# Kernel tuning notes

Measured on AMD Instinct MI355X. Metric: run time of the kernel, lower is better.

The kernel has to match this reference:

```python
import jax, jax.numpy as jnp
import numpy as np

EMBED_DIM = 1024
NUM_HEADS = 16
HEAD_DIM = EMBED_DIM // NUM_HEADS
SCALE = HEAD_DIM ** -0.5


def setup_inputs() -> dict:
    key = jax.random.key(0)
    k_x, k_qkv, k_w, k_b = jax.random.split(key, 4)
    B, N = 2, 2048
    x = jax.random.normal(k_x, (B, N, EMBED_DIM), dtype=jnp.float32)
    # nn.Linear weights stored as (out, in); init with small normal
    w_qkv = jax.random.normal(k_qkv, (3 * EMBED_DIM, EMBED_DIM), dtype=jnp.float32) * (EMBED_DIM ** -0.5)
    w_out = jax.random.normal(k_w, (EMBED_DIM, EMBED_DIM), dtype=jnp.float32) * (EMBED_DIM ** -0.5)
    b_out = jax.random.normal(k_b, (EMBED_DIM,), dtype=jnp.float32) * 0.02
    return {"x": x, "w_qkv": w_qkv, "w_out": w_out, "b_out": b_out}


def reference(x, w_qkv, w_out, b_out):
    B, N, _ = x.shape
    # qkv: (B, N, 3*E) -> (B, N, 3, H, Dh)
    qkv = jnp.einsum('bne,fe->bnf', x, w_qkv).reshape(B, N, 3, NUM_HEADS, HEAD_DIM)
    q, k, v = qkv[:, :, 0], qkv[:, :, 1], qkv[:, :, 2]
    scores = jnp.einsum('bnhd,bmhd->bhnm', q, k) * SCALE
    attn = jax.nn.softmax(scores, axis=-1)  # dropout is identity in eval mode
    out = jnp.einsum('bhnm,bmhd->bnhd', attn, v).reshape(B, N, EMBED_DIM)
    return jnp.einsum('bne,fe->bnf', out, w_out) + b_out
```

## Files before the change

kernel.cpp:

```cpp
#include <hip/hip_runtime.h>
#include <stdint.h>
#include <stddef.h>

#define SEQ   2048
#define BATCH 2
#define NTOK  (SEQ*BATCH)
#define EMB   1024
#define QKVN  3072
#define NH    16
#define HD    64

typedef __bf16 bf16x8 __attribute__((ext_vector_type(8)));
typedef float  f32x4  __attribute__((ext_vector_type(4)));

__device__ __forceinline__ unsigned short f2b(float f) {
  union { float f; uint32_t u; } v; v.f = f;
  uint32_t r = v.u + 0x7fffu + ((v.u >> 16) & 1u);
  return (unsigned short)(r >> 16);
}

#define GLOAD_LDS16(gp, lp)                                                    \
  __builtin_amdgcn_global_load_lds(                                            \
      (__attribute__((address_space(1))) void*)(gp),                           \
      (__attribute__((address_space(3))) void*)(lp), 16, 0, 0)

__global__ void cvt3_kernel(const float* __restrict__ x,
                            const float* __restrict__ wq,
                            const float* __restrict__ wo,
                            unsigned short* __restrict__ xb,
                            unsigned short* __restrict__ wqb,
                            unsigned short* __restrict__ wob) {
  int i = blockIdx.x * blockDim.x + threadIdx.x;
  const float* in; unsigned short* out; int k;
  if (i < 1048576)              { in = x;  out = xb;  k = i; }
  else if (i < 1048576+786432)  { in = wq; out = wqb; k = i - 1048576; }
  else                          { in = wo; out = wob; k = i - (1048576+786432); }
  float4 v = ((const float4*)in)[k];
  ushort4 o;
  o.x = f2b(v.x); o.y = f2b(v.y); o.z = f2b(v.z); o.w = f2b(v.w);
  ((ushort4*)out)[k] = o;
}

__global__ __launch_bounds__(256) void gemm_bt(
    const unsigned short* __restrict__ A,
    const unsigned short* __restrict__ B,
    unsigned short* __restrict__ Cb,
    float* __restrict__ Cf,
    const float* __restrict__ bias,
    unsigned short* __restrict__ vt,
    int M, int N, int K, int mode)
{
  __shared__ unsigned short As[3][128*32];
  __shared__ unsigned short Bs[3][128*32];

  const int tid  = threadIdx.x;
  const int wave = tid >> 6, lane = tid & 63;
  const int l16  = lane & 15, quad = lane >> 4;
  const int tm = blockIdx.x * 128, tn = blockIdx.y * 128;
  const int wm = (wave & 1) * 64,  wn = (wave >> 1) * 64;

  const int e0   = (wave*2 + 0)*512 + lane*8;
  const int e1   = (wave*2 + 1)*512 + lane*8;
  const int row0 = e0 >> 5, kk0a = e0 & 31;
  const int row1 = e1 >> 5, kk1a = e1 & 31;
  const int ld0  = (wave*2 + 0)*512;
  const int ld1  = (wave*2 + 1)*512;

#define GSTAGE(bf, k0s)                                                        \
  do {                                                                         \
    GLOAD_LDS16(A + (size_t)(tm + row0)*K + ((k0s) + kk0a), As[bf] + ld0);     \
    GLOAD_LDS16(B + (size_t)(tn + row0)*K + ((k0s) + kk0a), Bs[bf] + ld0);     \
    GLOAD_LDS16(A + (size_t)(tm + row1)*K + ((k0s) + kk1a), As[bf] + ld1);     \
    GLOAD_LDS16(B + (size_t)(tn + row1)*K + ((k0s) + kk1a), Bs[bf] + ld1);     \
  } while (0)

  f32x4 acc[4][4] = {};
  const int nst = K >> 5;

  GSTAGE(0, 0);
  GSTAGE(1, 32);

  int b0i = 0, b1i = 1, b2i = 2;
  for (int t = 0; t < nst; ++t) {
    if (t + 2 < nst) GSTAGE(b2i, (t + 2)*32);

    if (t + 2 < nst)      asm volatile("s_waitcnt vmcnt(8)" ::: "memory");
    else if (t + 1 < nst) asm volatile("s_waitcnt vmcnt(4)" ::: "memory");
    else                  asm volatile("s_waitcnt vmcnt(0)" ::: "memory");
    __builtin_amdgcn_s_barrier();
    __builtin_amdgcn_sched_barrier(0);

    const unsigned short* Ac = As[b0i];
    const unsigned short* Bc = Bs[b0i];
    bf16x8 af[4], bf[4];
#pragma unroll
    for (int i = 0; i < 4; ++i) {
      af[i] = *(const bf16x8*)(Ac + (wm + i*16 + l16)*32 + quad*8);
      bf[i] = *(const bf16x8*)(Bc + (wn + i*16 + l16)*32 + quad*8);
    }
#pragma unroll
    for (int mi = 0; mi < 4; ++mi)
#pragma unroll
      for (int ni = 0; ni < 4; ++ni)
        acc[mi][ni] = __builtin_amdgcn_mfma_f32_16x16x32_bf16(af[mi], bf[ni], acc[mi][ni], 0, 0, 0);

    __builtin_amdgcn_s_barrier();
    __builtin_amdgcn_sched_barrier(0);
    const int tmp = b0i; b0i = b1i; b1i = b2i; b2i = tmp;
  }
#undef GSTAGE

  if (mode == 1) {
#pragma unroll
    for (int mi = 0; mi < 4; ++mi)
#pragma unroll
      for (int ni = 0; ni < 4; ++ni)
#pragma unroll
        for (int r = 0; r < 4; ++r) {
          const int row = tm + wm + mi*16 + quad*4 + r;
          const int col = tn + wn + ni*16 + l16;
          Cf[(size_t)row*N + col] = acc[mi][ni][r] + bias[col];
        }
  } else {
    if (tn < 2048) {
#pragma unroll
      for (int mi = 0; mi < 4; ++mi)
#pragma unroll
        for (int ni = 0; ni < 4; ++ni)
#pragma unroll
          for (int r = 0; r < 4; ++r) {
            const int row = tm + wm + mi*16 + quad*4 + r;
            const int col = tn + wn + ni*16 + l16;
            Cb[(size_t)row*2048 + col] = f2b(acc[mi][ni][r]);
          }
    } else {
#pragma unroll
      for (int mi = 0; mi < 4; ++mi)
#pragma unroll
        for (int ni = 0; ni < 4; ++ni) {
          const int f     = tn + wn + ni*16 + l16 - 2048;
          const int row0_ = tm + wm + mi*16 + quad*4;
          const int bb    = row0_ >> 11;
          const int n0    = row0_ & 2047;
          ushort4 pv;
          pv.x = f2b(acc[mi][ni][0]); pv.y = f2b(acc[mi][ni][1]);
          pv.z = f2b(acc[mi][ni][2]); pv.w = f2b(acc[mi][ni][3]);
          *(ushort4*)(vt + ((size_t)(bb*1024 + f))*2048 + n0) = pv;
        }
    }
  }
}

__global__ __launch_bounds__(256) void attn_kernel(
    const unsigned short* __restrict__ qk,
    const unsigned short* __restrict__ vT,
    unsigned short* __restrict__ aout)
{
  __shared__ unsigned short Ks[4][32*64];
  __shared__ unsigned short Vt[4][64*32];

  const int tid  = threadIdx.x;
  const int wave = tid >> 6, lane = tid & 63;
  const int l16  = lane & 15, quad = lane >> 4;

  const int flat = blockIdx.x;
  const int xcd  = flat & 7;
  const int idx  = flat >> 3;
  const int bh   = xcd*4 + (idx >> 5);
  const int qt   = idx & 31;
  const int b  = bh >> 4, h = bh & 15;
  const size_t tok0 = (size_t)b * SEQ;
  const int qrow0 = qt*64 + wave*16;
  const int ksw = l16 & 7;
  const int xsw = (l16 >> 1) & 3;

  const int p     = wave*64 + lane;
  const int krow  = p >> 3;
  const int kc    = ((p & 7) ^ (krow & 7)) << 3;
  const int vd    = p >> 2;
  const int vc    = ((p & 3) ^ ((vd >> 1) & 3)) << 3;
  const unsigned short* kbase = qk + tok0*2048 + 1024 + h*64;
  const unsigned short* vbase = vT + ((size_t)(b*1024 + h*64))*2048;
  const int ldstw = wave*512;

#define STAGE(bf, t)                                                          \
  do {                                                                        \
    const int _kk = (t)*32;                                                   \
    GLOAD_LDS16(kbase + (size_t)(_kk + krow)*2048 + kc, &Ks[bf][ldstw]);      \
    GLOAD_LDS16(vbase + (size_t)vd*2048 + _kk + vc,     &Vt[bf][ldstw]);      \
  } while (0)

  const float LOG2E = 1.44269504f;
  const float OFF2  = 17.3123405f;
#define SM_TO_PF(sReg, pfOut, lAcc)                                            \
  do {                                                                         \
    uint32_t A0_, A1_, B0_, B1_;                                               \
    float rs_ = (lAcc);                                                        \
    _Pragma("unroll")                                                          \
    for (int mf_ = 0; mf_ < 2; ++mf_) {                                        \
      union { float f; uint32_t u; } a0, a1, a2, a3;                           \
      a0.f = __builtin_amdgcn_exp2f(fmaf((sReg)[mf_][0], LOG2E, -OFF2));       \
      a1.f = __builtin_amdgcn_exp2f(fmaf((sReg)[mf_][1], LOG2E, -OFF2));       \
      a2.f = __builtin_amdgcn_exp2f(fmaf((sReg)[mf_][2], LOG2E, -OFF2));       \
      a3.f = __builtin_amdgcn_exp2f(fmaf((sReg)[mf_][3], LOG2E, -OFF2));       \
      rs_ += (a0.f + a1.f) + (a2.f + a3.f);                                    \
      uint32_t w0 = __builtin_amdgcn_perm(a1.u, a0.u, 0x07060302u);            \
      uint32_t w1 = __builtin_amdgcn_perm(a3.u, a2.u, 0x07060302u);            \
      if (mf_ == 0) { A0_ = w0; A1_ = w1; } else { B0_ = w0; B1_ = w1; }       \
    }                                                                          \
    (lAcc) = rs_;                                                              \
    asm("v_permlane32_swap_b32 %0, %1" : "+v"(A0_), "+v"(B0_));                \
    asm("v_permlane32_swap_b32 %0, %1" : "+v"(A1_), "+v"(B1_));                \
    asm("v_permlane16_swap_b32 %0, %1" : "+v"(A0_), "+v"(B0_));                \
    asm("v_permlane16_swap_b32 %0, %1" : "+v"(A1_), "+v"(B1_));                \
    union { uint32_t u[4]; bf16x8 v; } pu_;                                    \
    pu_.u[0] = A0_; pu_.u[1] = A1_; pu_.u[2] = B0_; pu_.u[3] = B1_;            \
    (pfOut) = pu_.v;                                                           \
  } while (0)

  bf16x8 qf[2];
  {
    const unsigned short* qp = qk + (tok0 + qrow0 + l16)*2048 + h*64;
#pragma unroll
    for (int ks = 0; ks < 2; ++ks) {
      bf16x8 t = *(const bf16x8*)(qp + ks*32 + quad*8);
#pragma unroll
      for (int j = 0; j < 8; ++j) t[j] = (__bf16)((float)t[j] * 0.125f);
      qf[ks] = t;
    }
  }

  f32x4 oacc[4] = {};
  float l_run = 0.f;

  STAGE(0, 0);
  STAGE(1, 1);
  __syncthreads();

#pragma unroll 2
  for (int kbb = 0; kbb < SEQ/64; ++kbb) {
    const int t0 = kbb*2;
    const int b0 = t0 & 3, b1 = (t0 + 1) & 3;
    if (t0 + 2 < SEQ/32) { STAGE((t0+2)&3, t0+2); STAGE((t0+3)&3, t0+3); }

    f32x4 sA[2] = {}, sB[2] = {};
    __builtin_amdgcn_s_setprio(1);
#pragma unroll
    for (int ks = 0; ks < 2; ++ks)
#pragma unroll
      for (int mf = 0; mf < 2; ++mf) {
        bf16x8 kf = *(const bf16x8*)(&Ks[b0][(mf*16 + l16)*64 + (((ks*4 + quad) ^ ksw) << 3)]);
        sA[mf] = __builtin_amdgcn_mfma_f32_16x16x32_bf16(kf, qf[ks], sA[mf], 0, 0, 0);
      }
#pragma unroll
    for (int ks = 0; ks < 2; ++ks)
#pragma unroll
      for (int mf = 0; mf < 2; ++mf) {
        bf16x8 kf = *(const bf16x8*)(&Ks[b1][(mf*16 + l16)*64 + (((ks*4 + quad) ^ ksw) << 3)]);
        sB[mf] = __builtin_amdgcn_mfma_f32_16x16x32_bf16(kf, qf[ks], sB[mf], 0, 0, 0);
      }
    __builtin_amdgcn_s_setprio(0);

    bf16x8 pfA;
    SM_TO_PF(sA, pfA, l_run);
    __builtin_amdgcn_s_setprio(1);
#pragma unroll
    for (int mf = 0; mf < 4; ++mf) {
      bf16x8 vf = *(const bf16x8*)(&Vt[b0][(mf*16 + l16)*32 + ((quad ^ xsw) << 3)]);
      oacc[mf] = __builtin_amdgcn_mfma_f32_16x16x32_bf16(vf, pfA, oacc[mf], 0, 0, 0);
    }
    __builtin_amdgcn_s_setprio(0);

    bf16x8 pfB;
    SM_TO_PF(sB, pfB, l_run);
    __builtin_amdgcn_s_setprio(1);
#pragma unroll
    for (int mf = 0; mf < 4; ++mf) {
      bf16x8 vf = *(const bf16x8*)(&Vt[b1][(mf*16 + l16)*32 + ((quad ^ xsw) << 3)]);
      oacc[mf] = __builtin_amdgcn_mfma_f32_16x16x32_bf16(vf, pfB, oacc[mf], 0, 0, 0);
    }
    __builtin_amdgcn_s_setprio(0);

    __syncthreads();
  }
#undef STAGE
#undef SM_TO_PF

  {
    float l = l_run;
    l += __shfl_xor(l, 16);
    l += __shfl_xor(l, 32);
    const float inv = 1.0f / l;
    const size_t trow = tok0 + qrow0 + l16;
#pragma unroll
    for (int mf = 0; mf < 4; ++mf) {
      ushort4 ov;
      ov.x = f2b(oacc[mf][0] * inv);
      ov.y = f2b(oacc[mf][1] * inv);
      ov.z = f2b(oacc[mf][2] * inv);
      ov.w = f2b(oacc[mf][3] * inv);
      *(ushort4*)(aout + trow*EMB + h*64 + mf*16 + quad*4) = ov;
    }
  }
}

extern "C" void kernel_launch(void* const* d_in, const int* in_sizes, int n_in,
                              void* d_out, int out_size, void* d_ws, size_t ws_size,
                              hipStream_t stream) {
  const float* x     = (const float*)d_in[0];
  const float* w_qkv = (const float*)d_in[1];
  const float* w_out = (const float*)d_in[2];
  const float* b_out = (const float*)d_in[3];

  char* ws = (char*)d_ws;
  unsigned short* xb    = (unsigned short*)(ws);
  unsigned short* wqkvb = (unsigned short*)(ws + 8388608);
  unsigned short* woutb = (unsigned short*)(ws + 14680064);
  unsigned short* qkb   = (unsigned short*)(ws + 16777216);
  unsigned short* vTb   = (unsigned short*)(ws + 33554432);
  unsigned short* aob   = (unsigned short*)(ws + 41943040);

  cvt3_kernel<<<8192, 256, 0, stream>>>(x, w_qkv, w_out, xb, wqkvb, woutb);

  gemm_bt<<<dim3(NTOK/128, QKVN/128), 256, 0, stream>>>(
      xb, wqkvb, qkb, nullptr, nullptr, vTb, NTOK, QKVN, EMB, 2);

  attn_kernel<<<dim3(1024), 256, 0, stream>>>(qkb, vTb, aob);

  gemm_bt<<<dim3(NTOK/128, EMB/128), 256, 0, stream>>>(
      aob, woutb, nullptr, (float*)d_out, b_out, nullptr, NTOK, EMB, EMB, 1);
}
```

Measured before the change: 188.4 us.

## Use 256x256 tiles with 512 threads and XCD-aware mapping for QKV GEMM

Adds a dedicated QKV projection GEMM kernel with 256x256 output tiles, 8 waves of 128x64 each, and a block-index remap that groups work per XCD. The larger tile roughly halves global/LDS traffic per FLOP relative to 128x128 tiles and launches 192 workgroups, fewer than the 256 CUs on the device. The out-projection GEMM is simplified to a single fp32+bias epilogue. Risks include higher register pressure (128 accumulator floats per lane), 96KB of LDS per block limiting occupancy, and some CUs left idle.

```diff
diff --git a/kernel.cpp b/kernel.cpp
--- a/kernel.cpp
+++ b/kernel.cpp
@@ -41,14 +41,108 @@
   ((ushort4*)out)[k] = o;
 }
 
+__global__ __launch_bounds__(512) void gemm256_qkv(
+    const unsigned short* __restrict__ A,
+    const unsigned short* __restrict__ B,
+    unsigned short* __restrict__ Cb,
+    unsigned short* __restrict__ vt)
+{
+  __shared__ unsigned short As[3][256*32];
+  __shared__ unsigned short Bs[3][256*32];
+
+  const int tid  = threadIdx.x;
+  const int wave = tid >> 6, lane = tid & 63;
+  const int l16  = lane & 15, quad = lane >> 4;
+  const int K = 1024;
+
+  const int flat = blockIdx.x;
+  const int wg   = (flat & 7) * 24 + (flat >> 3);
+  const int mt   = wg & 15, nt = wg >> 4;
+  const int tm   = mt * 256, tn = nt * 256;
+  const int wm   = (wave >> 2) * 128;
+  const int wn   = (wave & 3) * 64;
+
+  const int p0 = tid,        r0 = p0 >> 2, c0 = (p0 & 3) << 3;
+  const int p1 = 512 + tid,  r1 = p1 >> 2, c1 = (p1 & 3) << 3;
+
+#define GSTAGE(bf, k0s)                                                        \
+  do {                                                                         \
+    GLOAD_LDS16(A + (size_t)(tm + r0)*K + ((k0s) + c0), As[bf] + wave*512);    \
+    GLOAD_LDS16(B + (size_t)(tn + r0)*K + ((k0s) + c0), Bs[bf] + wave*512);    \
+    GLOAD_LDS16(A + (size_t)(tm + r1)*K + ((k0s) + c1), As[bf] + 4096 + wave*512); \
+    GLOAD_LDS16(B + (size_t)(tn + r1)*K + ((k0s) + c1), Bs[bf] + 4096 + wave*512); \
+  } while (0)
+
+  f32x4 acc[8][4] = {};
+
+  GSTAGE(0, 0);
+  GSTAGE(1, 32);
+
+  int b0i = 0, b1i = 1, b2i = 2;
+  for (int t = 0; t < 32; ++t) {
+    if (t + 2 < 32) GSTAGE(b2i, (t + 2)*32);
+
+    if (t + 2 < 32)      asm volatile("s_waitcnt vmcnt(8)" ::: "memory");
+    else if (t + 1 < 32) asm volatile("s_waitcnt vmcnt(4)" ::: "memory");
+    else                 asm volatile("s_waitcnt vmcnt(0)" ::: "memory");
+    __builtin_amdgcn_s_barrier();
+    __builtin_amdgcn_sched_barrier(0);
+
+    const unsigned short* Ac = As[b0i];
+    const unsigned short* Bc = Bs[b0i];
+    bf16x8 af[8], bg[4];
+#pragma unroll
+    for (int i = 0; i < 8; ++i)
+      af[i] = *(const bf16x8*)(Ac + (wm + i*16 + l16)*32 + quad*8);
+#pragma unroll
+    for (int i = 0; i < 4; ++i)
+      bg[i] = *(const bf16x8*)(Bc + (wn + i*16 + l16)*32 + quad*8);
+#pragma unroll
+    for (int mi = 0; mi < 8; ++mi)
+#pragma unroll
+      for (int ni = 0; ni < 4; ++ni)
+        acc[mi][ni] = __builtin_amdgcn_mfma_f32_16x16x32_bf16(af[mi], bg[ni], acc[mi][ni], 0, 0, 0);
+
+    __builtin_amdgcn_s_barrier();
+    __builtin_amdgcn_sched_barrier(0);
+    const int tmp = b0i; b0i = b1i; b1i = b2i; b2i = tmp;
+  }
+#undef GSTAGE
+
+  if (tn < 2048) {
+#pragma unroll
+    for (int mi = 0; mi < 8; ++mi)
+#pragma unroll
+      for (int ni = 0; ni < 4; ++ni)
+#pragma unroll
+        for (int r = 0; r < 4; ++r) {
+          const int row = tm + wm + mi*16 + quad*4 + r;
+          const int col = tn + wn + ni*16 + l16;
+          Cb[(size_t)row*2048 + col] = f2b(acc[mi][ni][r]);
+        }
+  } else {
+#pragma unroll
+    for (int mi = 0; mi < 8; ++mi)
+#pragma unroll
+      for (int ni = 0; ni < 4; ++ni) {
+        const int f     = tn + wn + ni*16 + l16 - 2048;
+        const int row0_ = tm + wm + mi*16 + quad*4;
+        const int bb    = row0_ >> 11;
+        const int n0    = row0_ & 2047;
+        ushort4 pv;
+        pv.x = f2b(acc[mi][ni][0]); pv.y = f2b(acc[mi][ni][1]);
+        pv.z = f2b(acc[mi][ni][2]); pv.w = f2b(acc[mi][ni][3]);
+        *(ushort4*)(vt + ((size_t)(bb*1024 + f))*2048 + n0) = pv;
+      }
+  }
+}
+
 __global__ __launch_bounds__(256) void gemm_bt(
     const unsigned short* __restrict__ A,
     const unsigned short* __restrict__ B,
-    unsigned short* __restrict__ Cb,
     float* __restrict__ Cf,
     const float* __restrict__ bias,
-    unsigned short* __restrict__ vt,
-    int M, int N, int K, int mode)
+    int M, int N, int K)
 {
   __shared__ unsigned short As[3][128*32];
   __shared__ unsigned short Bs[3][128*32];
@@ -110,45 +204,16 @@
   }
 #undef GSTAGE
 
-  if (mode == 1) {
-#pragma unroll
-    for (int mi = 0; mi < 4; ++mi)
-#pragma unroll
-      for (int ni = 0; ni < 4; ++ni)
-#pragma unroll
-        for (int r = 0; r < 4; ++r) {
-          const int row = tm + wm + mi*16 + quad*4 + r;
-          const int col = tn + wn + ni*16 + l16;
-          Cf[(size_t)row*N + col] = acc[mi][ni][r] + bias[col];
-        }
-  } else {
-    if (tn < 2048) {
-#pragma unroll
-      for (int mi = 0; mi < 4; ++mi)
-#pragma unroll
-        for (int ni = 0; ni < 4; ++ni)
-#pragma unroll
-          for (int r = 0; r < 4; ++r) {
-            const int row = tm + wm + mi*16 + quad*4 + r;
-            const int col = tn + wn + ni*16 + l16;
-            Cb[(size_t)row*2048 + col] = f2b(acc[mi][ni][r]);
-          }
-    } else {
-#pragma unroll
-      for (int mi = 0; mi < 4; ++mi)
-#pragma unroll
-        for (int ni = 0; ni < 4; ++ni) {
-          const int f     = tn + wn + ni*16 + l16 - 2048;
-          const int row0_ = tm + wm + mi*16 + quad*4;
-          const int bb    = row0_ >> 11;
-          const int n0    = row0_ & 2047;
-          ushort4 pv;
-          pv.x = f2b(acc[mi][ni][0]); pv.y = f2b(acc[mi][ni][1]);
-          pv.z = f2b(acc[mi][ni][2]); pv.w = f2b(acc[mi][ni][3]);
-          *(ushort4*)(vt + ((size_t)(bb*1024 + f))*2048 + n0) = pv;
-        }
-    }
-  }
+#pragma unroll
+  for (int mi = 0; mi < 4; ++mi)
+#pragma unroll
+    for (int ni = 0; ni < 4; ++ni)
+#pragma unroll
+      for (int r = 0; r < 4; ++r) {
+        const int row = tm + wm + mi*16 + quad*4 + r;
+        const int col = tn + wn + ni*16 + l16;
+        Cf[(size_t)row*N + col] = acc[mi][ni][r] + bias[col];
+      }
 }
 
 __global__ __launch_bounds__(256) void attn_kernel(
@@ -322,11 +387,10 @@
 
   cvt3_kernel<<<8192, 256, 0, stream>>>(x, w_qkv, w_out, xb, wqkvb, woutb);
 
-  gemm_bt<<<dim3(NTOK/128, QKVN/128), 256, 0, stream>>>(
-      xb, wqkvb, qkb, nullptr, nullptr, vTb, NTOK, QKVN, EMB, 2);
+  gemm256_qkv<<<192, 512, 0, stream>>>(xb, wqkvb, qkb, vTb);
 
   attn_kernel<<<dim3(1024), 256, 0, stream>>>(qkb, vTb, aob);
 
   gemm_bt<<<dim3(NTOK/128, EMB/128), 256, 0, stream>>>(
-      aob, woutb, nullptr, (float*)d_out, b_out, nullptr, NTOK, EMB, EMB, 1);
-}
+      aob, woutb, (float*)d_out, b_out, NTOK, EMB, EMB);
+}
```

Measured after the change: 199.1 us. 1.06x slower.
